# Kernel optimization log

Hardware: AMD Instinct MI355X
Metric: run time of the kernel (lower is better)

The kernel has to match this reference:

```python
import jax, jax.numpy as jnp
import numpy as np

H = 16  # num_attention_heads

def setup_inputs() -> dict:
    key = jax.random.key(0)
    ks = jax.random.split(key, 4)
    B, S, D = 4, 2048, 1024
    scale = 1.0 / np.sqrt(D)
    return {
        "hidden_states": jax.random.normal(ks[0], (B, S, D), dtype=jnp.float32),
        "attention_mask": jnp.zeros((B, 1, 1, S), dtype=jnp.float32),
        "Wq": jax.random.normal(ks[1], (D, D), dtype=jnp.float32) * scale,
        "bq": jnp.zeros((D,), dtype=jnp.float32),
        "Wk": jax.random.normal(ks[2], (D, D), dtype=jnp.float32) * scale,
        "bk": jnp.zeros((D,), dtype=jnp.float32),
        "Wv": jax.random.normal(ks[3], (D, D), dtype=jnp.float32) * scale,
        "bv": jnp.zeros((D,), dtype=jnp.float32),
    }

def _split_heads(x, B, S):
    # [B,S,D] -> [B,H,S,Dh]
    return x.reshape(B, S, H, -1).transpose(0, 2, 1, 3)

def reference(hidden_states, attention_mask, Wq, bq, Wk, bk, Wv, bv):
    B, S, D = hidden_states.shape
    Dh = D // H
    q = _split_heads(hidden_states @ Wq.T + bq, B, S)  # [B,H,S,Dh]
    k = _split_heads(hidden_states @ Wk.T + bk, B, S)
    v = _split_heads(hidden_states @ Wv.T + bv, B, S)
    scores = jnp.einsum("bhqd,bhkd->bhqk", q, k) / jnp.sqrt(jnp.float32(Dh))
    scores = scores + attention_mask  # additive mask, broadcast [B,1,1,S]
    probs = jax.nn.softmax(scores, axis=-1)  # dropout is identity in eval mode
    ctx = jnp.einsum("bhqk,bhkd->bhqd", probs, v)  # [B,H,S,Dh]
    ctx = ctx.transpose(0, 2, 1, 3).reshape(B, S, D)
    return ctx
```

## Files before the change

### kernel.cpp

```cpp
#include <hip/hip_runtime.h>
#include <hip/hip_bf16.h>
#include <stdint.h>

#define LOG2E 1.44269504088896340736f
#define SCL   (0.125f * LOG2E)

typedef __attribute__((ext_vector_type(8)))  short short8;
typedef __attribute__((ext_vector_type(4)))  float floatx4;
typedef __attribute__((ext_vector_type(16))) float floatx16;
typedef __attribute__((ext_vector_type(4)))  unsigned short ushort4v;

#define GLP(g, l)                                                              \
    __builtin_amdgcn_global_load_lds(                                          \
        (const __attribute__((address_space(1))) void*)(g),                    \
        (__attribute__((address_space(3))) void*)(l), 16, 0, 0)

static __device__ __forceinline__ unsigned short f2bf(float f) {
    union { float f; unsigned u; } v; v.f = f;
    unsigned r = v.u + 0x7FFFu + ((v.u >> 16) & 1u);
    return (unsigned short)(r >> 16);
}

static __device__ __forceinline__ unsigned pack2bf(float a, float b) {
    __hip_bfloat162 h = __float22bfloat162_rn(make_float2(a, b));
    union { __hip_bfloat162 h; unsigned u; } c; c.h = h; return c.u;
}

__global__ __launch_bounds__(256) void cvt_kernel(const float* __restrict__ in,
                                                  unsigned short* __restrict__ out,
                                                  int n4) {
    int i = blockIdx.x * 256 + threadIdx.x;
    if (i < n4) {
        float4 v = ((const float4*)in)[i];
        ushort4v o;
        o.x = f2bf(v.x); o.y = f2bf(v.y); o.z = f2bf(v.z); o.w = f2bf(v.w);
        ((ushort4v*)out)[i] = o;
    }
}

__global__ __launch_bounds__(256) void cvt_w3m(const float* __restrict__ Wq,
                                               const float* __restrict__ Wk,
                                               const float* __restrict__ Wv,
                                               const float* __restrict__ mask,
                                               unsigned short* __restrict__ out,
                                               float* __restrict__ maskl) {
    int i = blockIdx.x * 256 + threadIdx.x;
    if (i < 786432) {
        const float* src; int j;
        if (i < 262144)      { src = Wq; j = i; }
        else if (i < 524288) { src = Wk; j = i - 262144; }
        else                 { src = Wv; j = i - 524288; }
        float4 v = ((const float4*)src)[j];
        ushort4v o;
        o.x = f2bf(v.x); o.y = f2bf(v.y); o.z = f2bf(v.z); o.w = f2bf(v.w);
        ((ushort4v*)out)[i] = o;
    } else if (i < 786432 + 2048) {
        int j = i - 786432;
        float4 v = ((const float4*)mask)[j];
        ((float4*)maskl)[j] = make_float4(v.x * LOG2E, v.y * LOG2E,
                                          v.z * LOG2E, v.w * LOG2E);
    }
}

__global__ __launch_bounds__(256) void qkv_gemm(
        const unsigned short* __restrict__ X,
        const unsigned short* __restrict__ W,
        const float* __restrict__ bq, const float* __restrict__ bk,
        const float* __restrict__ bv,
        unsigned short* __restrict__ Qf,
        unsigned short* __restrict__ Kf,
        unsigned short* __restrict__ Vt)
{
    __shared__ __align__(16) unsigned short sh[17408];
    unsigned short* Ash = sh;
    unsigned short* Bsh = sh + 8192;

    const int tid  = threadIdx.x;
    const int lane = tid & 63;
    const int wv   = tid >> 6;
    const int quad = lane >> 4;
    const int ln   = lane & 15;
    const int mBase = blockIdx.x * 128;
    const int nBase = blockIdx.y * 128;
    const int wm = (wv >> 1) * 64;
    const int wn = (wv & 1) * 64;

    floatx4 acc[4][4];
#pragma unroll
    for (int i = 0; i < 4; ++i)
#pragma unroll
        for (int j = 0; j < 4; ++j) acc[i][j] = 0.0f;

    const int sr = lane >> 3;
    const int kc = (lane & 7) ^ sr;

    for (int kb = 0; kb < 1024; kb += 64) {
        __syncthreads();
#pragma unroll
        for (int s = 0; s < 4; ++s) {
            const int seg = wv * 4 + s;
            const int row = seg * 8 + sr;
            GLP(X + (size_t)(mBase + row) * 1024 + kb + kc * 8, Ash + seg * 512);
            GLP(W + (size_t)(nBase + row) * 1024 + kb + kc * 8, Bsh + seg * 512);
        }
        __syncthreads();
#pragma unroll
        for (int kk = 0; kk < 2; ++kk) {
            const int c = kk * 4 + quad;
            short8 aF[4], bF[4];
#pragma unroll
            for (int i = 0; i < 4; ++i) {
                const int R = wm + i * 16 + ln;
                aF[i] = *(const short8*)(Ash + (R >> 3) * 512 + (R & 7) * 64 + ((c ^ (R & 7)) * 8));
            }
#pragma unroll
            for (int j = 0; j < 4; ++j) {
                const int R = wn + j * 16 + ln;
                bF[j] = *(const short8*)(Bsh + (R >> 3) * 512 + (R & 7) * 64 + ((c ^ (R & 7)) * 8));
            }
#pragma unroll
            for (int i = 0; i < 4; ++i)
#pragma unroll
                for (int j = 0; j < 4; ++j)
                    acc[i][j] = __builtin_amdgcn_mfma_f32_16x16x32_bf16(
                        aF[i], bF[j], acc[i][j], 0, 0, 0);
        }
    }

    if (blockIdx.y < 16) {
        unsigned short* dst = (blockIdx.y < 8) ? Qf : Kf;
        const float* bias   = (blockIdx.y < 8) ? bq : bk;
        const int nb = nBase & 1023;
        float bj[4];
#pragma unroll
        for (int j = 0; j < 4; ++j)
            bj[j] = bias[nb + wn + j * 16 + ln];
        __syncthreads();
#pragma unroll
        for (int j = 0; j < 4; ++j) {
            const int col = wn + j * 16 + ln;
#pragma unroll
            for (int i = 0; i < 4; ++i) {
                const int row0 = wm + i * 16 + quad * 4;
#pragma unroll
                for (int r = 0; r < 4; ++r)
                    sh[(row0 + r) * 136 + col] = f2bf(acc[i][j][r] + bj[j]);
            }
        }
        __syncthreads();
#pragma unroll
        for (int it = 0; it < 8; ++it) {
            const int row  = it * 16 + (tid >> 4);
            const int part = tid & 15;
            short8 v = *(const short8*)(sh + row * 136 + part * 8);
            *(short8*)(dst + (size_t)(mBase + row) * 1024 + nb + part * 8) = v;
        }
    } else {
#pragma unroll
        for (int j = 0; j < 4; ++j) {
            const int gn = nBase + wn + j * 16 + ln;
            const int c  = gn & 1023;
            const int h  = c >> 6;
            const int d  = c & 63;
            const float bias = bv[c];
#pragma unroll
            for (int i = 0; i < 4; ++i) {
                const int gm0 = mBase + wm + i * 16 + quad * 4;
                const int b   = gm0 >> 11;
                const int s0  = gm0 & 2047;
                ushort4v pv;
#pragma unroll
                for (int r = 0; r < 4; ++r) pv[r] = f2bf(acc[i][j][r] + bias);
                *(ushort4v*)(Vt + (size_t)((b * 16 + h) * 64 + d) * 2048 + s0) = pv;
            }
        }
    }
}

__global__ __launch_bounds__(256) void attn_kernel(
        const unsigned short* __restrict__ Qf,
        const unsigned short* __restrict__ Kf,
        const unsigned short* __restrict__ VT,
        const float* __restrict__ maskl,
        float* __restrict__ out)
{
    __shared__ __align__(16) unsigned short Ksh[64 * 64];
    __shared__ __align__(16) unsigned short Vsh[64 * 64];
    __shared__ __align__(16) unsigned short Psh[4 * 32 * 72];
    __shared__ __align__(16) float Msh[256];

    const int tid  = threadIdx.x;
    const int lane = tid & 63;
    const int wv   = tid >> 6;
    const int q32  = lane & 31;
    const int hi   = lane >> 5;
    const int bh   = blockIdx.x & 63;
    const int qt   = blockIdx.x >> 6;
    const int b    = bh >> 4;
    const int h    = bh & 15;
    const int q0   = qt * 128 + wv * 32;

    short8 bQ[4];
#pragma unroll
    for (int ks = 0; ks < 4; ++ks)
        bQ[ks] = *(const short8*)(Qf + (size_t)(b * 2048 + q0 + q32) * 1024
                                     + h * 64 + ks * 16 + hi * 8);
    short8 ones;
#pragma unroll
    for (int j = 0; j < 8; ++j) ones[j] = (short)0x3F80;

    floatx16 accO0 = 0.0f, accO1 = 0.0f, accL = 0.0f;

    const int sr = lane >> 3;
    const int kc = (lane & 7) ^ sr;
    const unsigned short* gK = Kf + (size_t)(b * 2048) * 1024 + h * 64;
    const unsigned short* gV = VT + (size_t)(bh * 64) * 2048;
    const float* mrow = maskl + b * 2048;
    unsigned short* pw = Psh + wv * (32 * 72);

    for (int kb = 0; kb < 2048; kb += 64) {
        __syncthreads();
#pragma unroll
        for (int s = 0; s < 2; ++s) {
            const int row = wv * 16 + s * 8 + sr;
            GLP(gK + (size_t)(kb + row) * 1024 + kc * 8, Ksh + (wv * 16 + s * 8) * 64);
            GLP(gV + (size_t)row * 2048 + kb + kc * 8,  Vsh + (wv * 16 + s * 8) * 64);
        }
        if (tid < 16) GLP(mrow + kb + lane * 4, Msh);
        __syncthreads();

#pragma unroll
        for (int mt = 0; mt < 2; ++mt) {
            floatx16 sacc = 0.0f;
#pragma unroll
            for (int ks = 0; ks < 4; ++ks) {
                const int row  = mt * 32 + q32;
                const int slot = (2 * ks + hi) ^ (row & 7);
                short8 aK = *(const short8*)(Ksh + row * 64 + slot * 8);
                sacc = __builtin_amdgcn_mfma_f32_32x32x16_bf16(aK, bQ[ks], sacc, 0, 0, 0);
            }
#pragma unroll
            for (int g = 0; g < 4; ++g) {
                const int key0 = mt * 32 + g * 8 + hi * 4;
                float4 mv4 = *(const float4*)(Msh + key0);
                float p0 = exp2f(sacc[g * 4 + 0] * SCL + mv4.x);
                float p1 = exp2f(sacc[g * 4 + 1] * SCL + mv4.y);
                float p2 = exp2f(sacc[g * 4 + 2] * SCL + mv4.z);
                float p3 = exp2f(sacc[g * 4 + 3] * SCL + mv4.w);
                *(uint2*)(pw + q32 * 72 + key0) =
                    make_uint2(pack2bf(p0, p1), pack2bf(p2, p3));
            }
        }

#pragma unroll
        for (int ks = 0; ks < 4; ++ks) {
            short8 aP = *(const short8*)(pw + q32 * 72 + ks * 16 + hi * 8);
            const int slot = (2 * ks + hi) ^ (q32 & 7);
            short8 bV0 = *(const short8*)(Vsh + q32 * 64 + slot * 8);
            short8 bV1 = *(const short8*)(Vsh + (32 + q32) * 64 + slot * 8);
            accO0 = __builtin_amdgcn_mfma_f32_32x32x16_bf16(aP, bV0, accO0, 0, 0, 0);
            accO1 = __builtin_amdgcn_mfma_f32_32x32x16_bf16(aP, bV1, accO1, 0, 0, 0);
            accL  = __builtin_amdgcn_mfma_f32_32x32x16_bf16(aP, ones, accL, 0, 0, 0);
        }
    }

#pragma unroll
    for (int g = 0; g < 4; ++g)
#pragma unroll
        for (int rr = 0; rr < 4; ++rr) {
            const int r   = g * 4 + rr;
            const int row = rr + 8 * g + 4 * hi;
            const float linv = 1.0f / accL[r];
            float* op = out + (size_t)(b * 2048 + q0 + row) * 1024 + h * 64 + q32;
            op[0]  = accO0[r] * linv;
            op[32] = accO1[r] * linv;
        }
}

extern "C" void kernel_launch(void* const* d_in, const int* in_sizes, int n_in,
                              void* d_out, int out_size, void* d_ws, size_t ws_size,
                              hipStream_t stream) {
    const float* X    = (const float*)d_in[0];
    const float* mask = (const float*)d_in[1];
    const float* Wq   = (const float*)d_in[2];
    const float* bq   = (const float*)d_in[3];
    const float* Wk   = (const float*)d_in[4];
    const float* bk   = (const float*)d_in[5];
    const float* Wv   = (const float*)d_in[6];
    const float* bv   = (const float*)d_in[7];
    float* out = (float*)d_out;

    char* ws = (char*)d_ws;
    unsigned short* xb  = (unsigned short*)(ws);
    unsigned short* wb  = (unsigned short*)(ws + 16777216);
    unsigned short* qf  = (unsigned short*)(ws + 23068672);
    unsigned short* kf  = (unsigned short*)(ws + 39845888);
    unsigned short* vtb = (unsigned short*)(ws + 56623104);
    float*          ml  = (float*)(ws + 73400320);

    cvt_kernel<<<8192, 256, 0, stream>>>(X, xb, 2097152);
    cvt_w3m<<<3080, 256, 0, stream>>>(Wq, Wk, Wv, mask, wb, ml);

    qkv_gemm<<<dim3(64, 24), 256, 0, stream>>>(xb, wb, bq, bk, bv, qf, kf, vtb);

    attn_kernel<<<1024, 256, 0, stream>>>(qf, kf, vtb, ml, out);
}
```

Measured before the change: 296.1 us.

## Double key tile per barrier, swizzle P buffer, use native exp2

```diff
diff --git a/kernel.cpp b/kernel.cpp
--- a/kernel.cpp
+++ b/kernel.cpp
@@ -14,6 +14,12 @@
     __builtin_amdgcn_global_load_lds(                                          \
         (const __attribute__((address_space(1))) void*)(g),                    \
         (__attribute__((address_space(3))) void*)(l), 16, 0, 0)
+
+#if __has_builtin(__builtin_amdgcn_exp2f)
+#define EXP2(x) __builtin_amdgcn_exp2f(x)
+#else
+#define EXP2(x) exp2f(x)
+#endif
 
 static __device__ __forceinline__ unsigned short f2bf(float f) {
     union { float f; unsigned u; } v; v.f = f;
@@ -184,10 +190,10 @@
         const float* __restrict__ maskl,
         float* __restrict__ out)
 {
-    __shared__ __align__(16) unsigned short Ksh[64 * 64];
-    __shared__ __align__(16) unsigned short Vsh[64 * 64];
-    __shared__ __align__(16) unsigned short Psh[4 * 32 * 72];
-    __shared__ __align__(16) float Msh[256];
+    __shared__ __align__(16) unsigned short Ksh[128 * 64];
+    __shared__ __align__(16) unsigned short Vsh[64 * 128];
+    __shared__ __align__(16) unsigned short Psh[4 * 32 * 64];
+    __shared__ __align__(16) float Msh[128];
 
     const int tid  = threadIdx.x;
     const int lane = tid & 63;
@@ -199,6 +205,7 @@
     const int b    = bh >> 4;
     const int h    = bh & 15;
     const int q0   = qt * 128 + wv * 32;
+    const int sw   = q32 & 7;
 
     short8 bQ[4];
 #pragma unroll
@@ -211,56 +218,67 @@
 
     floatx16 accO0 = 0.0f, accO1 = 0.0f, accL = 0.0f;
 
-    const int sr = lane >> 3;
-    const int kc = (lane & 7) ^ sr;
     const unsigned short* gK = Kf + (size_t)(b * 2048) * 1024 + h * 64;
     const unsigned short* gV = VT + (size_t)(bh * 64) * 2048;
     const float* mrow = maskl + b * 2048;
-    unsigned short* pw = Psh + wv * (32 * 72);
-
-    for (int kb = 0; kb < 2048; kb += 64) {
-        __syncthreads();
-#pragma unroll
-        for (int s = 0; s < 2; ++s) {
-            const int row = wv * 16 + s * 8 + sr;
-            GLP(gK + (size_t)(kb + row) * 1024 + kc * 8, Ksh + (wv * 16 + s * 8) * 64);
-            GLP(gV + (size_t)row * 2048 + kb + kc * 8,  Vsh + (wv * 16 + s * 8) * 64);
-        }
-        if (tid < 16) GLP(mrow + kb + lane * 4, Msh);
-        __syncthreads();
-
-#pragma unroll
-        for (int mt = 0; mt < 2; ++mt) {
-            floatx16 sacc = 0.0f;
+    unsigned short* pw = Psh + wv * (32 * 64);
+
+    const int krr = lane >> 3;
+    const int kcs = lane & 7;
+    const int vrr = lane >> 4;
+    const int vcs = lane & 15;
+
+    for (int kb = 0; kb < 2048; kb += 128) {
+        __syncthreads();
+#pragma unroll
+        for (int s = 0; s < 4; ++s) {
+            const int seg = wv * 4 + s;
+            const int rK  = seg * 8 + krr;
+            const int cK  = kcs ^ (rK & 7);
+            GLP(gK + (size_t)(kb + rK) * 1024 + cK * 8, Ksh + seg * 512);
+            const int rV  = seg * 4 + vrr;
+            const int cV  = vcs ^ (rV & 7);
+            GLP(gV + (size_t)rV * 2048 + kb + cV * 8, Vsh + seg * 512);
+        }
+        if (tid < 32) GLP(mrow + kb + lane * 4, Msh);
+        __syncthreads();
+
+#pragma unroll
+        for (int half = 0; half < 2; ++half) {
+#pragma unroll
+            for (int mt = 0; mt < 2; ++mt) {
+                floatx16 sacc = 0.0f;
+#pragma unroll
+                for (int ks = 0; ks < 4; ++ks) {
+                    const int row  = half * 64 + mt * 32 + q32;
+                    const int slot = (2 * ks + hi) ^ sw;
+                    short8 aK = *(const short8*)(Ksh + row * 64 + slot * 8);
+                    sacc = __builtin_amdgcn_mfma_f32_32x32x16_bf16(aK, bQ[ks], sacc, 0, 0, 0);
+                }
+#pragma unroll
+                for (int g = 0; g < 4; ++g) {
+                    const int key0 = mt * 32 + g * 8 + hi * 4;
+                    float4 mv4 = *(const float4*)(Msh + half * 64 + key0);
+                    float p0 = EXP2(sacc[g * 4 + 0] * SCL + mv4.x);
+                    float p1 = EXP2(sacc[g * 4 + 1] * SCL + mv4.y);
+                    float p2 = EXP2(sacc[g * 4 + 2] * SCL + mv4.z);
+                    float p3 = EXP2(sacc[g * 4 + 3] * SCL + mv4.w);
+                    *(uint2*)(pw + q32 * 64 + (((mt * 4 + g) ^ sw) * 8) + hi * 4) =
+                        make_uint2(pack2bf(p0, p1), pack2bf(p2, p3));
+                }
+            }
+
 #pragma unroll
             for (int ks = 0; ks < 4; ++ks) {
-                const int row  = mt * 32 + q32;
-                const int slot = (2 * ks + hi) ^ (row & 7);
-                short8 aK = *(const short8*)(Ksh + row * 64 + slot * 8);
-                sacc = __builtin_amdgcn_mfma_f32_32x32x16_bf16(aK, bQ[ks], sacc, 0, 0, 0);
-            }
-#pragma unroll
-            for (int g = 0; g < 4; ++g) {
-                const int key0 = mt * 32 + g * 8 + hi * 4;
-                float4 mv4 = *(const float4*)(Msh + key0);
-                float p0 = exp2f(sacc[g * 4 + 0] * SCL + mv4.x);
-                float p1 = exp2f(sacc[g * 4 + 1] * SCL + mv4.y);
-                float p2 = exp2f(sacc[g * 4 + 2] * SCL + mv4.z);
-                float p3 = exp2f(sacc[g * 4 + 3] * SCL + mv4.w);
-                *(uint2*)(pw + q32 * 72 + key0) =
-                    make_uint2(pack2bf(p0, p1), pack2bf(p2, p3));
-            }
-        }
-
-#pragma unroll
-        for (int ks = 0; ks < 4; ++ks) {
-            short8 aP = *(const short8*)(pw + q32 * 72 + ks * 16 + hi * 8);
-            const int slot = (2 * ks + hi) ^ (q32 & 7);
-            short8 bV0 = *(const short8*)(Vsh + q32 * 64 + slot * 8);
-            short8 bV1 = *(const short8*)(Vsh + (32 + q32) * 64 + slot * 8);
-            accO0 = __builtin_amdgcn_mfma_f32_32x32x16_bf16(aP, bV0, accO0, 0, 0, 0);
-            accO1 = __builtin_amdgcn_mfma_f32_32x32x16_bf16(aP, bV1, accO1, 0, 0, 0);
-            accL  = __builtin_amdgcn_mfma_f32_32x32x16_bf16(aP, ones, accL, 0, 0, 0);
+                const int cs = (2 * ks + hi) ^ sw;
+                short8 aP  = *(const short8*)(pw + q32 * 64 + cs * 8);
+                const int cv = half * 8 + cs;
+                short8 bV0 = *(const short8*)(Vsh + q32 * 128 + cv * 8);
+                short8 bV1 = *(const short8*)(Vsh + (32 + q32) * 128 + cv * 8);
+                accO0 = __builtin_amdgcn_mfma_f32_32x32x16_bf16(aP, bV0, accO0, 0, 0, 0);
+                accO1 = __builtin_amdgcn_mfma_f32_32x32x16_bf16(aP, bV1, accO1, 0, 0, 0);
+                accL  = __builtin_amdgcn_mfma_f32_32x32x16_bf16(aP, ones, accL, 0, 0, 0);
+            }
         }
     }
 
```

Measured after the change: 272.8 us. -7.9%, faster.
